# Performance work log

Hardware: AMD Instinct MI355X
Metric: run time of the kernel (lower is better)

Reference implementation:

```python
import jax, jax.numpy as jnp
import numpy as np

N_NODES = 200000
N_EVENTS = 100000
MEM_DIM = 100
TIME_DIM = 100
MSG_DIM = 172
T_MAX = 1000000


def setup_inputs() -> dict:
    key = jax.random.key(0)
    ks = jax.random.split(key, 12)
    s = 0.05
    return {
        "memory": jax.random.normal(ks[0], (N_NODES, MEM_DIM), jnp.float32),
        "raw_msg": jax.random.normal(ks[1], (N_EVENTS, MSG_DIM), jnp.float32),
        "time_w": jax.random.normal(ks[2], (TIME_DIM, 1), jnp.float32) * s,
        "time_b": jax.random.normal(ks[3], (TIME_DIM,), jnp.float32) * s,
        "w_ih": jax.random.normal(ks[4], (3 * MEM_DIM, 2 * MEM_DIM + MSG_DIM + TIME_DIM), jnp.float32) * s,
        "w_hh": jax.random.normal(ks[5], (3 * MEM_DIM, MEM_DIM), jnp.float32) * s,
        "b_ih": jax.random.normal(ks[6], (3 * MEM_DIM,), jnp.float32) * s,
        "b_hh": jax.random.normal(ks[7], (3 * MEM_DIM,), jnp.float32) * s,
        "last_update": jax.random.randint(ks[8], (N_NODES,), 0, T_MAX, jnp.int32),
        "src": jax.random.randint(ks[9], (N_EVENTS,), 0, N_NODES, jnp.int32),
        "dst": jax.random.randint(ks[10], (N_EVENTS,), 0, N_NODES, jnp.int32),
        "t": jax.random.randint(ks[11], (N_EVENTS,), 0, T_MAX, jnp.int32),
    }


def _time_enc(t_rel, time_w, time_b):
    # Linear(1, time_dim) followed by cos, as in TGN.update_memory
    return jnp.cos(t_rel[:, None] * time_w[:, 0][None, :] + time_b[None, :])


def _gru_cell(x, h, w_ih, w_hh, b_ih, b_hh):
    gi = x @ w_ih.T + b_ih  # [N, 3*D]
    gh = h @ w_hh.T + b_hh
    i_r, i_z, i_n = jnp.split(gi, 3, axis=-1)
    h_r, h_z, h_n = jnp.split(gh, 3, axis=-1)
    r = jax.nn.sigmoid(i_r + h_r)
    z = jax.nn.sigmoid(i_z + h_z)
    n = jnp.tanh(i_n + r * h_n)
    return (1.0 - z) * n + z * h


def reference(memory, raw_msg, time_w, time_b, w_ih, w_hh, b_ih, b_hh,
              last_update, src, dst, t):
    # time-relative encodings for source- and destination-side messages
    t_rel_s = (t - last_update[src]).astype(memory.dtype)
    t_rel_d = (t - last_update[dst]).astype(memory.dtype)
    t_enc_s = _time_enc(t_rel_s, time_w, time_b)  # [E, time_dim]
    t_enc_d = _time_enc(t_rel_d, time_w, time_b)

    mem_s = memory[src]  # [E, D]
    mem_d = memory[dst]

    # IdentityMessage: concat(mem_self, mem_other, raw_msg, t_enc)
    msg_s = jnp.concatenate([mem_s, mem_d, raw_msg, t_enc_s], axis=-1)  # [E, 472]
    msg_d = jnp.concatenate([mem_d, mem_s, raw_msg, t_enc_d], axis=-1)

    idx = jnp.concatenate([src, dst], axis=0)          # [2E]
    msgs = jnp.concatenate([msg_s, msg_d], axis=0)      # [2E, 472]

    n_nodes = memory.shape[0]
    # MeanAggregator: per-node mean of incoming messages
    summed = jax.ops.segment_sum(msgs, idx, num_segments=n_nodes)  # [N, 472]
    counts = jax.ops.segment_sum(jnp.ones((idx.shape[0],), memory.dtype), idx,
                                 num_segments=n_nodes)             # [N]
    aggr = summed / jnp.maximum(counts, 1.0)[:, None]

    # GRU memory update, applied only to nodes that received messages
    h_new = _gru_cell(aggr, memory, w_ih, w_hh, b_ih, b_hh)
    touched = (counts > 0)[:, None]
    return jnp.where(touched, h_new, memory)  # [N, memory_dim]
```

## Files before the change

kernel.cpp:

```cpp
#include <hip/hip_runtime.h>
#include <math.h>

#define NND 200000
#define NEV 100000
#define MD 100
#define TD 100
#define MSGD 172
#define NB 64
#define NFRAG 25
#define KS 15
#define BP_ELEMS (KS * NFRAG * 64 * 8)
#define GLS 74

typedef __attribute__((ext_vector_type(8))) short bf16x8;
typedef __attribute__((ext_vector_type(4))) float f32x4;

__device__ __forceinline__ float fast_sigmoid(float x) {
    return 1.0f / (1.0f + __expf(-x));
}
__device__ __forceinline__ float fast_tanh(float x) {
    return fmaf(2.0f, 1.0f / (1.0f + __expf(-2.0f * x)), -1.0f);
}

__device__ __forceinline__ unsigned short f2bf(float f) {
    union { float f; unsigned int u; } v; v.f = f;
    unsigned int r = (v.u + 0x7FFFu + ((v.u >> 16) & 1u)) >> 16;
    return (unsigned short)r;
}
__device__ __forceinline__ float bf2f(unsigned int h) {
    union { unsigned int u; float f; } v; v.u = h << 16;
    return v.f;
}
__device__ __forceinline__ unsigned int pk(float a, float b) {
    unsigned int r;
    asm("v_cvt_pk_bf16_f32 %0, %1, %2" : "=v"(r) : "v"(a), "v"(b));
    return r;
}

__global__ __launch_bounds__(256) void k_count(
    const int* __restrict__ src, const int* __restrict__ dst, int* __restrict__ cnt)
{
    int e = blockIdx.x * 256 + threadIdx.x;
    if (e >= NEV) return;
    atomicAdd(&cnt[src[e]], 1);
    atomicAdd(&cnt[dst[e]], 1);
}

__global__ __launch_bounds__(256) void k_scan1(
    const int* __restrict__ cnt, int* __restrict__ off, int* __restrict__ tpos,
    int* __restrict__ psum, int* __restrict__ psumC)
{
    __shared__ int s[5][256];
    int t = threadIdx.x, b = blockIdx.x;
    int i0 = b * 1024 + t * 4;
    int v[4], cls[4];
#pragma unroll
    for (int j = 0; j < 4; ++j) {
        v[j] = (i0 + j < NND) ? cnt[i0 + j] : 0;
        cls[j] = (v[j] == 0) ? -1 : ((v[j] < 4 ? v[j] : 4) - 1);
    }
    int tsum = v[0] + v[1] + v[2] + v[3];
    int fs[4] = {0, 0, 0, 0};
#pragma unroll
    for (int j = 0; j < 4; ++j)
        if (cls[j] >= 0) fs[cls[j]]++;
    s[0][t] = tsum;
#pragma unroll
    for (int X = 0; X < 4; ++X) s[1 + X][t] = fs[X];
    __syncthreads();
    for (int o = 1; o < 256; o <<= 1) {
        int x[5];
#pragma unroll
        for (int ch = 0; ch < 5; ++ch) x[ch] = (t >= o) ? s[ch][t - o] : 0;
        __syncthreads();
#pragma unroll
        for (int ch = 0; ch < 5; ++ch) s[ch][t] += x[ch];
        __syncthreads();
    }
    int e0 = s[0][t] - tsum;
    int eC[4];
#pragma unroll
    for (int X = 0; X < 4; ++X) eC[X] = s[1 + X][t] - fs[X];
    int run = 0;
    int cseen[4] = {0, 0, 0, 0};
#pragma unroll
    for (int j = 0; j < 4; ++j) {
        int i = i0 + j;
        if (i < NND) {
            off[i] = e0 + run;
            if (cls[j] >= 0) tpos[i] = eC[cls[j]] + cseen[cls[j]];
        }
        run += v[j];
        if (cls[j] >= 0) cseen[cls[j]]++;
    }
    if (t == 255) {
        psum[b] = s[0][255];
#pragma unroll
        for (int X = 0; X < 4; ++X) psumC[X * 256 + b] = s[1 + X][255];
    }
}

__global__ __launch_bounds__(256) void k_scan2(
    int* __restrict__ psum, int* __restrict__ psumC,
    int* __restrict__ clsBase, int* __restrict__ ntp, int nblk)
{
    __shared__ int s[5][256];
    int t = threadIdx.x;
    int v[5];
    v[0] = (t < nblk) ? psum[t] : 0;
#pragma unroll
    for (int X = 0; X < 4; ++X) v[1 + X] = (t < nblk) ? psumC[X * 256 + t] : 0;
#pragma unroll
    for (int ch = 0; ch < 5; ++ch) s[ch][t] = v[ch];
    __syncthreads();
    for (int o = 1; o < 256; o <<= 1) {
        int x[5];
#pragma unroll
        for (int ch = 0; ch < 5; ++ch) x[ch] = (t >= o) ? s[ch][t - o] : 0;
        __syncthreads();
#pragma unroll
        for (int ch = 0; ch < 5; ++ch) s[ch][t] += x[ch];
        __syncthreads();
    }
    if (t < nblk) {
        psum[t] = s[0][t] - v[0];
#pragma unroll
        for (int X = 0; X < 4; ++X) psumC[X * 256 + t] = s[1 + X][t] - v[1 + X];
    }
    if (t == 0) {
        int T0 = s[1][nblk - 1], T1 = s[2][nblk - 1];
        int T2 = s[3][nblk - 1], T3 = s[4][nblk - 1];
        clsBase[0] = 0;
        clsBase[1] = T0;
        clsBase[2] = T0 + T1;
        clsBase[3] = T0 + T1 + T2;
        ntp[0] = T0 + T1 + T2 + T3;
    }
}

__global__ __launch_bounds__(256) void k_scan3(
    const int* __restrict__ cnt, int* __restrict__ off, int* __restrict__ tpos,
    const int* __restrict__ psum, const int* __restrict__ psumC,
    const int* __restrict__ clsBase, int* __restrict__ cur)
{
    int t = threadIdx.x, b = blockIdx.x;
    int base = psum[b];
    int i0 = b * 1024 + t * 4;
#pragma unroll
    for (int j = 0; j < 4; ++j) {
        int i = i0 + j;
        if (i < NND) {
            int v = off[i] + base;
            off[i] = v;
            cur[i] = v;
            int c = cnt[i];
            if (c > 0) {
                int cls = (c < 4 ? c : 4) - 1;
                tpos[i] = clsBase[cls] + psumC[cls * 256 + b] + tpos[i];
            }
        }
    }
}

__global__ __launch_bounds__(256) void k_copytouch(
    const float* __restrict__ memory, const int* __restrict__ cnt,
    const int* __restrict__ off, const int* __restrict__ tpos,
    float* __restrict__ out, int4* __restrict__ tinfo)
{
    int idx = blockIdx.x * 256 + threadIdx.x;
    if (idx >= NND * 25) return;
    int node = idx / 25, u = idx - node * 25;
    int c = cnt[node];
    if (c == 0) {
        reinterpret_cast<float4*>(out)[idx] =
            reinterpret_cast<const float4*>(memory)[idx];
    } else if (u == 0) {
        tinfo[tpos[node]] = make_int4(node, c, off[node], 0);
    }
}

__global__ __launch_bounds__(256) void k_place(
    const int* __restrict__ src, const int* __restrict__ dst,
    const int* __restrict__ tarr, const int* __restrict__ last_update,
    int* __restrict__ cur, int4* __restrict__ entries)
{
    int e = blockIdx.x * 256 + threadIdx.x;
    if (e >= NEV) return;
    int s = src[e], d = dst[e], tt = tarr[e];
    int slot = atomicAdd(&cur[s], 1);
    entries[slot] = make_int4(d, e, __float_as_int((float)(tt - last_update[s])), s);
    slot = atomicAdd(&cur[d], 1);
    entries[slot] = make_int4(s, e, __float_as_int((float)(tt - last_update[d])), d);
}

__global__ __launch_bounds__(256) void k_convert(
    const float* __restrict__ w_ih, const float* __restrict__ w_hh,
    const float* __restrict__ memory, const float* __restrict__ raw_msg,
    unsigned short* __restrict__ Bp, uint4* __restrict__ membf,
    uint4* __restrict__ rawbf)
{
    int idx = blockIdx.x * 256 + threadIdx.x;
    if (idx < BP_ELEMS) {
        int e = idx & 7;
        int lane = (idx >> 3) & 63;
        int t = idx >> 9;
        int nf = t % 25;
        int ks = t / 25;
        int col = nf * 16 + (lane & 15);
        int k = ks * 32 + ((lane >> 4) << 3) + e;
        float v = 0.0f;
        if (col < 200) {
            if (k < 472) v = w_ih[col * 472 + k];
            if (k < 100) v += w_hh[col * 100 + k];
        } else if (col < 300) {
            if (k < 472) v = w_ih[col * 472 + k];
        } else {
            if (k < 100) v = w_hh[(col - 100) * 100 + k];
        }
        Bp[idx] = f2bf(v);
        return;
    }
    int j = idx - BP_ELEMS;
    if (j < NND * 13) {
        int node = j / 13, u = j - node * 13;
        const float4* ms = reinterpret_cast<const float4*>(memory + (size_t)node * MD);
        uint4 o = (uint4){0u, 0u, 0u, 0u};
        if (u < 12) {
            float4 x = ms[2 * u], y = ms[2 * u + 1];
            o.x = pk(x.x, x.y); o.y = pk(x.z, x.w);
            o.z = pk(y.x, y.y); o.w = pk(y.z, y.w);
        } else {
            float4 x = ms[24];
            o.x = pk(x.x, x.y); o.y = pk(x.z, x.w);
        }
        membf[j] = o;
        return;
    }
    j -= NND * 13;
    if (j < NEV * 22) {
        int e = j / 22, r = j - e * 22;
        const float4* rs = reinterpret_cast<const float4*>(raw_msg + (size_t)e * MSGD);
        float4 x = rs[2 * r];
        float4 y = (float4){0.f, 0.f, 0.f, 0.f};
        if (2 * r + 1 < 43) y = rs[2 * r + 1];
        uint4 o;
        o.x = pk(x.x, x.y); o.y = pk(x.z, x.w);
        o.z = pk(y.x, y.y); o.w = pk(y.z, y.w);
        rawbf[j] = o;
    }
}

__global__ __launch_bounds__(512, 4) void tgn_gemm(
    const uint4* __restrict__ membf,
    const uint4* __restrict__ rawbf, const int4* __restrict__ entries,
    const float* __restrict__ time_w, const float* __restrict__ time_b,
    const unsigned short* __restrict__ Bp,
    const float* __restrict__ b_ih, const float* __restrict__ b_hh,
    const int* __restrict__ ntp, const int4* __restrict__ tinfo,
    float* __restrict__ out)
{
    __shared__ __align__(16) unsigned short lds[64 * 480];
    __shared__ int node_s[NB], cnt_s[NB], off_s[NB];
    int tid = threadIdx.x;
    int n0 = blockIdx.x * NB;
    int nt = ntp[0];
    if (n0 >= nt) return;

    if (tid < NB) {
        int slot = n0 + tid;
        if (slot < nt) {
            int4 ti = tinfo[slot];
            node_s[tid] = ti.x; cnt_s[tid] = ti.y; off_s[tid] = ti.z;
        } else {
            node_s[tid] = -1; cnt_s[tid] = 0; off_s[tid] = 0;
        }
    }
    __syncthreads();

    int lane = tid & 63;
    int wv = tid >> 6;

    {
        int u = lane;
        bool lOther = (u >= 13 && u <= 24);
        bool lRaw   = (u >= 25 && u <= 45);
        bool lMix   = (u == 12);
        bool lR46   = (u == 46);
        bool lTenc  = (u >= 47 && u <= 58);
        int offA = lOther ? (16 * u - 200) : (16 * u - 400);

        float tw[8], tb[8];
#pragma unroll
        for (int j = 0; j < 8; ++j) { tw[j] = 0.f; tb[j] = 0.f; }
        if (lTenc) {
            int d0 = 8 * u - 372;
            float4 wa = *reinterpret_cast<const float4*>(time_w + d0);
            float4 wb = *reinterpret_cast<const float4*>(time_w + d0 + 4);
            float4 ba = *reinterpret_cast<const float4*>(time_b + d0);
            float4 bb = *reinterpret_cast<const float4*>(time_b + d0 + 4);
            tw[0] = wa.x; tw[1] = wa.y; tw[2] = wa.z; tw[3] = wa.w;
            tw[4] = wb.x; tw[5] = wb.y; tw[6] = wb.z; tw[7] = wb.w;
            tb[0] = ba.x; tb[1] = ba.y; tb[2] = ba.z; tb[3] = ba.w;
            tb[4] = bb.x; tb[5] = bb.y; tb[6] = bb.z; tb[7] = bb.w;
        } else if (lR46) {
            float4 wa = *reinterpret_cast<const float4*>(time_w);
            float4 ba = *reinterpret_cast<const float4*>(time_b);
            tw[4] = wa.x; tw[5] = wa.y; tw[6] = wa.z; tw[7] = wa.w;
            tb[4] = ba.x; tb[5] = ba.y; tb[6] = ba.z; tb[7] = ba.w;
        }

        const char* membc = reinterpret_cast<const char*>(membf);
        const char* rawbc = reinterpret_cast<const char*>(rawbf);

#pragma unroll
        for (int half = 0; half < 2; ++half) {
            int rb = wv * 8 + half * 4;
            int cc[4], oo[4];
#pragma unroll
            for (int r = 0; r < 4; ++r) { cc[r] = cnt_s[rb + r]; oo[r] = off_s[rb + r]; }
            int maxc = max(max(cc[0], cc[1]), max(cc[2], cc[3]));
            int4 en[4];
#pragma unroll
            for (int r = 0; r < 4; ++r)
                en[r] = (cc[r] > 0) ? entries[oo[r]] : make_int4(0, 0, 0, 0);
            uint4 mreg[4];
#pragma unroll
            for (int r = 0; r < 4; ++r) {
                int nd = node_s[rb + r];
                mreg[r] = (u < 13 && nd >= 0) ? membf[(size_t)nd * 13 + u]
                                              : (uint4){0u, 0u, 0u, 0u};
            }
            uint2 gA[4], gB[4];
#pragma unroll
            for (int r = 0; r < 4; ++r) {
                gA[r] = (uint2){0u, 0u}; gB[r] = (uint2){0u, 0u};
                if (cc[r] > 0) {
                    if (lOther) {
                        const char* p = membc + (size_t)en[r].x * 208 + offA;
                        gA[r] = *reinterpret_cast<const uint2*>(p);
                        gB[r] = *reinterpret_cast<const uint2*>(p + 8);
                    } else if (lMix) {
                        gB[r] = *reinterpret_cast<const uint2*>(membc + (size_t)en[r].x * 208);
                    } else if (lRaw) {
                        const char* p = rawbc + (size_t)en[r].y * 352 + offA;
                        gA[r] = *reinterpret_cast<const uint2*>(p);
                        gB[r] = *reinterpret_cast<const uint2*>(p + 8);
                    } else if (lR46) {
                        gA[r] = *reinterpret_cast<const uint2*>(rawbc + (size_t)en[r].y * 352 + 336);
                    }
                }
            }
            float ac[4][8];
#pragma unroll
            for (int r = 0; r < 4; ++r) {
                ac[r][0] = bf2f(gA[r].x & 0xffffu); ac[r][1] = bf2f(gA[r].x >> 16);
                ac[r][2] = bf2f(gA[r].y & 0xffffu); ac[r][3] = bf2f(gA[r].y >> 16);
                ac[r][4] = bf2f(gB[r].x & 0xffffu); ac[r][5] = bf2f(gB[r].x >> 16);
                ac[r][6] = bf2f(gB[r].y & 0xffffu); ac[r][7] = bf2f(gB[r].y >> 16);
                if ((lTenc || lR46) && cc[r] > 0) {
                    float trel = __int_as_float(en[r].z);
                    if (lTenc) {
                        ac[r][0] = __cosf(fmaf(trel, tw[0], tb[0]));
                        ac[r][1] = __cosf(fmaf(trel, tw[1], tb[1]));
                        ac[r][2] = __cosf(fmaf(trel, tw[2], tb[2]));
                        ac[r][3] = __cosf(fmaf(trel, tw[3], tb[3]));
                    }
                    ac[r][4] = __cosf(fmaf(trel, tw[4], tb[4]));
                    ac[r][5] = __cosf(fmaf(trel, tw[5], tb[5]));
                    ac[r][6] = __cosf(fmaf(trel, tw[6], tb[6]));
                    ac[r][7] = __cosf(fmaf(trel, tw[7], tb[7]));
                }
            }
            for (int j = 1; j < maxc; ++j) {
                int4 e2[4];
#pragma unroll
                for (int r = 0; r < 4; ++r) {
                    int slot = oo[r] + ((j < cc[r]) ? j : 0);
                    e2[r] = entries[slot];
                }
                uint2 hA[4], hB[4];
#pragma unroll
                for (int r = 0; r < 4; ++r) {
                    hA[r] = (uint2){0u, 0u}; hB[r] = (uint2){0u, 0u};
                    if (j < cc[r]) {
                        if (lOther) {
                            const char* p = membc + (size_t)e2[r].x * 208 + offA;
                            hA[r] = *reinterpret_cast<const uint2*>(p);
                            hB[r] = *reinterpret_cast<const uint2*>(p + 8);
                        } else if (lMix) {
                            hB[r] = *reinterpret_cast<const uint2*>(membc + (size_t)e2[r].x * 208);
                        } else if (lRaw) {
                            const char* p = rawbc + (size_t)e2[r].y * 352 + offA;
                            hA[r] = *reinterpret_cast<const uint2*>(p);
                            hB[r] = *reinterpret_cast<const uint2*>(p + 8);
                        } else if (lR46) {
                            hA[r] = *reinterpret_cast<const uint2*>(rawbc + (size_t)e2[r].y * 352 + 336);
                        }
                    }
                }
#pragma unroll
                for (int r = 0; r < 4; ++r) {
                    if (j < cc[r]) {
                        ac[r][0] += bf2f(hA[r].x & 0xffffu); ac[r][1] += bf2f(hA[r].x >> 16);
                        ac[r][2] += bf2f(hA[r].y & 0xffffu); ac[r][3] += bf2f(hA[r].y >> 16);
                        ac[r][4] += bf2f(hB[r].x & 0xffffu); ac[r][5] += bf2f(hB[r].x >> 16);
                        ac[r][6] += bf2f(hB[r].y & 0xffffu); ac[r][7] += bf2f(hB[r].y >> 16);
                        if (lTenc || lR46) {
                            float trel = __int_as_float(e2[r].z);
                            if (lTenc) {
                                ac[r][0] += __cosf(fmaf(trel, tw[0], tb[0]));
                                ac[r][1] += __cosf(fmaf(trel, tw[1], tb[1]));
                                ac[r][2] += __cosf(fmaf(trel, tw[2], tb[2]));
                                ac[r][3] += __cosf(fmaf(trel, tw[3], tb[3]));
                            }
                            ac[r][4] += __cosf(fmaf(trel, tw[4], tb[4]));
                            ac[r][5] += __cosf(fmaf(trel, tw[5], tb[5]));
                            ac[r][6] += __cosf(fmaf(trel, tw[6], tb[6]));
                            ac[r][7] += __cosf(fmaf(trel, tw[7], tb[7]));
                        }
                    }
                }
            }
#pragma unroll
            for (int r = 0; r < 4; ++r) {
                float ci = 1.0f / fmaxf((float)cc[r], 1.0f);
                uint4 o;
                if (u < 12) {
                    o = mreg[r];
                } else {
                    o.x = (u == 12) ? mreg[r].x : pk(ac[r][0] * ci, ac[r][1] * ci);
                    o.y = (u == 12) ? mreg[r].y : pk(ac[r][2] * ci, ac[r][3] * ci);
                    o.z = pk(ac[r][4] * ci, ac[r][5] * ci);
                    o.w = pk(ac[r][6] * ci, ac[r][7] * ci);
                }
                if (u < 60) {
                    int nl = rb + r;
                    int byte = (nl * 960 + 16 * u) ^ ((nl & 7) << 4);
                    *reinterpret_cast<uint4*>(reinterpret_cast<char*>(lds) + byte) = o;
                }
            }
        }
    }
    __syncthreads();

    int l15 = lane & 15;
    int kg8 = (lane >> 4) << 3;
    int f0 = (wv == 0) ? 0 : (4 + 3 * (wv - 1));
    int cw = (wv == 0) ? 4 : 3;

    f32x4 acc[4][4];
#pragma unroll
    for (int g = 0; g < 4; ++g)
#pragma unroll
        for (int i = 0; i < 4; ++i) acc[g][i] = (f32x4){0.f, 0.f, 0.f, 0.f};

    const bf16x8* BpB = reinterpret_cast<const bf16x8*>(Bp);
    const char* ldsc = reinterpret_cast<const char*>(lds);

#pragma unroll
    for (int ks = 0; ks < KS; ++ks) {
        int k0 = ks * 32 + kg8;
        const bf16x8* bp = BpB + ((size_t)(ks * NFRAG + f0)) * 64 + lane;
        bf16x8 b[4];
#pragma unroll
        for (int i = 0; i < 4; ++i)
            if (i < cw) b[i] = bp[i * 64];
#pragma unroll
        for (int g = 0; g < 4; ++g) {
            int r = g * 16 + l15;
            int ab = (r * 960 + 2 * k0) ^ ((r & 7) << 4);
            bf16x8 a = *reinterpret_cast<const bf16x8*>(ldsc + ab);
#pragma unroll
            for (int i = 0; i < 4; ++i)
                if (i < cw)
                    acc[g][i] = __builtin_amdgcn_mfma_f32_16x16x32_bf16(a, b[i], acc[g][i], 0, 0, 0);
        }
    }

    float mv[13];
    {
        const char* membc = reinterpret_cast<const char*>(membf);
#pragma unroll
        for (int t = 0; t < 13; ++t) {
            int idx = tid + t * 512;
            mv[t] = 0.f;
            if (idx < NB * MD) {
                int n = idx / MD, j = idx - n * MD;
                int nd = node_s[n];
                if (nd >= 0) {
                    unsigned short h = *reinterpret_cast<const unsigned short*>(
                        membc + (size_t)nd * 208 + 2 * j);
                    mv[t] = bf2f((unsigned int)h);
                }
            }
        }
    }

    __syncthreads();

    unsigned short* Gl = lds;
    int kq = (lane >> 4) << 2;
#pragma unroll
    for (int i = 0; i < 4; ++i) {
        if (i < cw) {
            int col = (f0 + i) * 16 + l15;
            float bias = (col < 200) ? (b_ih[col] + b_hh[col])
                       : (col < 300) ? b_ih[col] : b_hh[col - 100];
#pragma unroll
            for (int g = 0; g < 4; ++g) {
                int node = g * 16 + kq;
#pragma unroll
                for (int rp = 0; rp < 2; ++rp) {
                    *reinterpret_cast<unsigned int*>(&Gl[col * GLS + node + 2 * rp]) =
                        pk(acc[g][i][2 * rp] + bias, acc[g][i][2 * rp + 1] + bias);
                }
            }
        }
    }
    __syncthreads();

#pragma unroll
    for (int t = 0; t < 13; ++t) {
        int idx = tid + t * 512;
        if (idx < NB * MD) {
            int n = idx / MD, j = idx - n * MD;
            int nd = node_s[n];
            if (nd >= 0) {
                float rp = bf2f((unsigned int)Gl[j * GLS + n]);
                float zp = bf2f((unsigned int)Gl[(100 + j) * GLS + n]);
                float inp = bf2f((unsigned int)Gl[(200 + j) * GLS + n]);
                float hnp = bf2f((unsigned int)Gl[(300 + j) * GLS + n]);
                float r = fast_sigmoid(rp);
                float z = fast_sigmoid(zp);
                float nn = fast_tanh(fmaf(r, hnp, inp));
                float h = (1.0f - z) * nn + z * mv[t];
                out[(size_t)nd * MD + j] = h;
            }
        }
    }
}

extern "C" void kernel_launch(void* const* d_in, const int* in_sizes, int n_in,
                              void* d_out, int out_size, void* d_ws, size_t ws_size,
                              hipStream_t stream)
{
    const float* memory      = (const float*)d_in[0];
    const float* raw_msg     = (const float*)d_in[1];
    const float* time_w      = (const float*)d_in[2];
    const float* time_b      = (const float*)d_in[3];
    const float* w_ih        = (const float*)d_in[4];
    const float* w_hh        = (const float*)d_in[5];
    const float* b_ih        = (const float*)d_in[6];
    const float* b_hh        = (const float*)d_in[7];
    const int*   last_update = (const int*)d_in[8];
    const int*   src         = (const int*)d_in[9];
    const int*   dst         = (const int*)d_in[10];
    const int*   tarr        = (const int*)d_in[11];
    float* out = (float*)d_out;

    int* cnt     = (int*)d_ws;
    int* off     = cnt + NND;
    int* cur     = off + NND;
    int* tpos    = cur + NND;
    int* psum    = tpos + NND;
    int* psumC   = psum + 256;
    int* clsBase = psumC + 1024;
    int* ntp     = clsBase + 4;
    int4* entries = (int4*)(ntp + 4);
    int4* tinfo = entries + 2 * NEV;
    uint4* membf = (uint4*)(tinfo + NND);
    uint4* rawbf = membf + (size_t)NND * 13;
    unsigned short* Bp = (unsigned short*)(rawbf + (size_t)NEV * 22);
    size_t need = (size_t)((char*)(Bp + BP_ELEMS) - (char*)d_ws);
    if (ws_size < need) return;

    const int NBLK = (NND + 1023) / 1024;
    const int NTILE = NND / NB;
    const int CVT_TOTAL = BP_ELEMS + NND * 13 + NEV * 22;

    hipMemsetAsync(cnt, 0, NND * sizeof(int), stream);
    k_convert<<<(CVT_TOTAL + 255) / 256, 256, 0, stream>>>(w_ih, w_hh, memory, raw_msg,
                                                           Bp, membf, rawbf);
    k_count<<<(NEV + 255) / 256, 256, 0, stream>>>(src, dst, cnt);
    k_scan1<<<NBLK, 256, 0, stream>>>(cnt, off, tpos, psum, psumC);
    k_scan2<<<1, 256, 0, stream>>>(psum, psumC, clsBase, ntp, NBLK);
    k_scan3<<<NBLK, 256, 0, stream>>>(cnt, off, tpos, psum, psumC, clsBase, cur);
    k_copytouch<<<(NND * 25 + 255) / 256, 256, 0, stream>>>(memory, cnt, off, tpos, out, tinfo);
    k_place<<<(NEV + 255) / 256, 256, 0, stream>>>(src, dst, tarr, last_update, cur, entries);
    tgn_gemm<<<NTILE, 512, 0, stream>>>(membf, rawbf, entries, time_w, time_b,
                                        Bp, b_ih, b_hh, ntp, tinfo, out);
}
```

Before: 256.6 us.

## Precompute time encodings per entry and merge copy/place kernels

Merges the copy-untouched and place-entries kernels into one launch. Adds a separate kernel that computes the bf16 time encoding for every entry slot, so the GEMM kernel gathers it like the other message parts. The gather code becomes a uniform per-lane source selection, and a fast path for tiles where every node has at most one message writes the gathered bf16 straight to LDS without float accumulation. The cost is an extra launch and 40 MB of extra workspace writes and reads for the encodings.

```diff
diff --git a/kernel.cpp b/kernel.cpp
--- a/kernel.cpp
+++ b/kernel.cpp
@@ -162,35 +162,48 @@
     }
 }
 
-__global__ __launch_bounds__(256) void k_copytouch(
+__global__ __launch_bounds__(256) void k_placecopy(
     const float* __restrict__ memory, const int* __restrict__ cnt,
     const int* __restrict__ off, const int* __restrict__ tpos,
-    float* __restrict__ out, int4* __restrict__ tinfo)
-{
-    int idx = blockIdx.x * 256 + threadIdx.x;
-    if (idx >= NND * 25) return;
-    int node = idx / 25, u = idx - node * 25;
-    int c = cnt[node];
-    if (c == 0) {
-        reinterpret_cast<float4*>(out)[idx] =
-            reinterpret_cast<const float4*>(memory)[idx];
-    } else if (u == 0) {
-        tinfo[tpos[node]] = make_int4(node, c, off[node], 0);
-    }
-}
-
-__global__ __launch_bounds__(256) void k_place(
     const int* __restrict__ src, const int* __restrict__ dst,
     const int* __restrict__ tarr, const int* __restrict__ last_update,
-    int* __restrict__ cur, int4* __restrict__ entries)
-{
-    int e = blockIdx.x * 256 + threadIdx.x;
-    if (e >= NEV) return;
-    int s = src[e], d = dst[e], tt = tarr[e];
-    int slot = atomicAdd(&cur[s], 1);
-    entries[slot] = make_int4(d, e, __float_as_int((float)(tt - last_update[s])), s);
-    slot = atomicAdd(&cur[d], 1);
-    entries[slot] = make_int4(s, e, __float_as_int((float)(tt - last_update[d])), d);
+    int* __restrict__ cur, float* __restrict__ out,
+    int4* __restrict__ tinfo, int4* __restrict__ entries)
+{
+    int idx = blockIdx.x * 256 + threadIdx.x;
+    if (idx < NND * 25) {
+        int node = idx / 25, u = idx - node * 25;
+        int c = cnt[node];
+        if (c == 0) {
+            reinterpret_cast<float4*>(out)[idx] =
+                reinterpret_cast<const float4*>(memory)[idx];
+        } else if (u == 0) {
+            tinfo[tpos[node]] = make_int4(node, c, off[node], 0);
+        }
+        return;
+    }
+    int e = idx - NND * 25;
+    if (e < NEV) {
+        int s = src[e], d = dst[e], tt = tarr[e];
+        int slot = atomicAdd(&cur[s], 1);
+        entries[slot] = make_int4(d, e, __float_as_int((float)(tt - last_update[s])), s);
+        slot = atomicAdd(&cur[d], 1);
+        entries[slot] = make_int4(s, e, __float_as_int((float)(tt - last_update[d])), d);
+    }
+}
+
+__global__ __launch_bounds__(256) void k_tenc(
+    const int4* __restrict__ entries, const float* __restrict__ time_w,
+    const float* __restrict__ time_b, unsigned int* __restrict__ tencbf)
+{
+    int slot = blockIdx.x * 2 + (threadIdx.x >> 7);
+    int k = threadIdx.x & 127;
+    if (k >= 50) return;
+    float trel = __int_as_float(entries[slot].z);
+    float2 w = *reinterpret_cast<const float2*>(time_w + 2 * k);
+    float2 b = *reinterpret_cast<const float2*>(time_b + 2 * k);
+    tencbf[(size_t)slot * 50 + k] =
+        pk(__cosf(fmaf(trel, w.x, b.x)), __cosf(fmaf(trel, w.y, b.y)));
 }
 
 __global__ __launch_bounds__(256) void k_convert(
@@ -251,9 +264,8 @@
 }
 
 __global__ __launch_bounds__(512, 4) void tgn_gemm(
-    const uint4* __restrict__ membf,
-    const uint4* __restrict__ rawbf, const int4* __restrict__ entries,
-    const float* __restrict__ time_w, const float* __restrict__ time_b,
+    const uint4* __restrict__ membf, const uint4* __restrict__ rawbf,
+    const unsigned int* __restrict__ tencbf, const int4* __restrict__ entries,
     const unsigned short* __restrict__ Bp,
     const float* __restrict__ b_ih, const float* __restrict__ b_hh,
     const int* __restrict__ ntp, const int4* __restrict__ tinfo,
@@ -282,35 +294,22 @@
 
     {
         int u = lane;
-        bool lOther = (u >= 13 && u <= 24);
-        bool lRaw   = (u >= 25 && u <= 45);
-        bool lMix   = (u == 12);
-        bool lR46   = (u == 46);
-        bool lTenc  = (u >= 47 && u <= 58);
-        int offA = lOther ? (16 * u - 200) : (16 * u - 400);
-
-        float tw[8], tb[8];
-#pragma unroll
-        for (int j = 0; j < 8; ++j) { tw[j] = 0.f; tb[j] = 0.f; }
-        if (lTenc) {
-            int d0 = 8 * u - 372;
-            float4 wa = *reinterpret_cast<const float4*>(time_w + d0);
-            float4 wb = *reinterpret_cast<const float4*>(time_w + d0 + 4);
-            float4 ba = *reinterpret_cast<const float4*>(time_b + d0);
-            float4 bb = *reinterpret_cast<const float4*>(time_b + d0 + 4);
-            tw[0] = wa.x; tw[1] = wa.y; tw[2] = wa.z; tw[3] = wa.w;
-            tw[4] = wb.x; tw[5] = wb.y; tw[6] = wb.z; tw[7] = wb.w;
-            tb[0] = ba.x; tb[1] = ba.y; tb[2] = ba.z; tb[3] = ba.w;
-            tb[4] = bb.x; tb[5] = bb.y; tb[6] = bb.z; tb[7] = bb.w;
-        } else if (lR46) {
-            float4 wa = *reinterpret_cast<const float4*>(time_w);
-            float4 ba = *reinterpret_cast<const float4*>(time_b);
-            tw[4] = wa.x; tw[5] = wa.y; tw[6] = wa.z; tw[7] = wa.w;
-            tb[4] = ba.x; tb[5] = ba.y; tb[6] = ba.z; tb[7] = ba.w;
-        }
-
         const char* membc = reinterpret_cast<const char*>(membf);
         const char* rawbc = reinterpret_cast<const char*>(rawbf);
+        const char* tencbc = reinterpret_cast<const char*>(tencbf);
+        int selA = 3, selB = 3, strA = 0, strB = 0;
+        const char* bA = membc;
+        const char* bB = membc;
+        if (u == 12) { selB = 0; strB = 208; bB = membc; }
+        else if (u >= 13 && u <= 24) { selA = selB = 0; strA = strB = 208; bA = membc + 16 * u - 200; bB = bA + 8; }
+        else if (u >= 25 && u <= 45) { selA = selB = 1; strA = strB = 352; bA = rawbc + 16 * u - 400; bB = bA + 8; }
+        else if (u == 46) { selA = 1; strA = 352; bA = rawbc + 336; selB = 2; strB = 200; bB = tencbc; }
+        else if (u >= 47 && u <= 58) { selA = selB = 2; strA = strB = 200; bA = tencbc + 16 * u - 744; bB = bA + 8; }
+        bool enA = (selA != 3), enB = (selB != 3);
+
+        auto gidx = [](int sel, int4 e, int slotId) {
+            return (sel == 0) ? e.x : ((sel == 1) ? e.y : slotId);
+        };
 
 #pragma unroll
         for (int half = 0; half < 2; ++half) {
@@ -335,108 +334,80 @@
             for (int r = 0; r < 4; ++r) {
                 gA[r] = (uint2){0u, 0u}; gB[r] = (uint2){0u, 0u};
                 if (cc[r] > 0) {
-                    if (lOther) {
-                        const char* p = membc + (size_t)en[r].x * 208 + offA;
-                        gA[r] = *reinterpret_cast<const uint2*>(p);
-                        gB[r] = *reinterpret_cast<const uint2*>(p + 8);
-                    } else if (lMix) {
-                        gB[r] = *reinterpret_cast<const uint2*>(membc + (size_t)en[r].x * 208);
-                    } else if (lRaw) {
-                        const char* p = rawbc + (size_t)en[r].y * 352 + offA;
-                        gA[r] = *reinterpret_cast<const uint2*>(p);
-                        gB[r] = *reinterpret_cast<const uint2*>(p + 8);
-                    } else if (lR46) {
-                        gA[r] = *reinterpret_cast<const uint2*>(rawbc + (size_t)en[r].y * 352 + 336);
+                    if (enA) gA[r] = *reinterpret_cast<const uint2*>(
+                        bA + (size_t)gidx(selA, en[r], oo[r]) * strA);
+                    if (enB) gB[r] = *reinterpret_cast<const uint2*>(
+                        bB + (size_t)gidx(selB, en[r], oo[r]) * strB);
+                }
+            }
+            if (maxc <= 1) {
+#pragma unroll
+                for (int r = 0; r < 4; ++r) {
+                    uint4 o;
+                    if (u < 12)       o = mreg[r];
+                    else if (u == 12) o = (uint4){mreg[r].x, mreg[r].y, gB[r].x, gB[r].y};
+                    else              o = (uint4){gA[r].x, gA[r].y, gB[r].x, gB[r].y};
+                    if (u < 60) {
+                        int nl = rb + r;
+                        int byte = (nl * 960 + 16 * u) ^ ((nl & 7) << 4);
+                        *reinterpret_cast<uint4*>(reinterpret_cast<char*>(lds) + byte) = o;
                     }
                 }
-            }
-            float ac[4][8];
-#pragma unroll
-            for (int r = 0; r < 4; ++r) {
-                ac[r][0] = bf2f(gA[r].x & 0xffffu); ac[r][1] = bf2f(gA[r].x >> 16);
-                ac[r][2] = bf2f(gA[r].y & 0xffffu); ac[r][3] = bf2f(gA[r].y >> 16);
-                ac[r][4] = bf2f(gB[r].x & 0xffffu); ac[r][5] = bf2f(gB[r].x >> 16);
-                ac[r][6] = bf2f(gB[r].y & 0xffffu); ac[r][7] = bf2f(gB[r].y >> 16);
-                if ((lTenc || lR46) && cc[r] > 0) {
-                    float trel = __int_as_float(en[r].z);
-                    if (lTenc) {
-                        ac[r][0] = __cosf(fmaf(trel, tw[0], tb[0]));
-                        ac[r][1] = __cosf(fmaf(trel, tw[1], tb[1]));
-                        ac[r][2] = __cosf(fmaf(trel, tw[2], tb[2]));
-                        ac[r][3] = __cosf(fmaf(trel, tw[3], tb[3]));
+            } else {
+                float ac[4][8];
+#pragma unroll
+                for (int r = 0; r < 4; ++r) {
+                    ac[r][0] = bf2f(gA[r].x & 0xffffu); ac[r][1] = bf2f(gA[r].x >> 16);
+                    ac[r][2] = bf2f(gA[r].y & 0xffffu); ac[r][3] = bf2f(gA[r].y >> 16);
+                    ac[r][4] = bf2f(gB[r].x & 0xffffu); ac[r][5] = bf2f(gB[r].x >> 16);
+                    ac[r][6] = bf2f(gB[r].y & 0xffffu); ac[r][7] = bf2f(gB[r].y >> 16);
+                }
+                for (int j = 1; j < maxc; ++j) {
+                    int sl[4];
+                    int4 e2[4];
+#pragma unroll
+                    for (int r = 0; r < 4; ++r) {
+                        sl[r] = oo[r] + ((j < cc[r]) ? j : 0);
+                        e2[r] = entries[sl[r]];
                     }
-                    ac[r][4] = __cosf(fmaf(trel, tw[4], tb[4]));
-                    ac[r][5] = __cosf(fmaf(trel, tw[5], tb[5]));
-                    ac[r][6] = __cosf(fmaf(trel, tw[6], tb[6]));
-                    ac[r][7] = __cosf(fmaf(trel, tw[7], tb[7]));
-                }
-            }
-            for (int j = 1; j < maxc; ++j) {
-                int4 e2[4];
-#pragma unroll
-                for (int r = 0; r < 4; ++r) {
-                    int slot = oo[r] + ((j < cc[r]) ? j : 0);
-                    e2[r] = entries[slot];
-                }
-                uint2 hA[4], hB[4];
-#pragma unroll
-                for (int r = 0; r < 4; ++r) {
-                    hA[r] = (uint2){0u, 0u}; hB[r] = (uint2){0u, 0u};
-                    if (j < cc[r]) {
-                        if (lOther) {
-                            const char* p = membc + (size_t)e2[r].x * 208 + offA;
-                            hA[r] = *reinterpret_cast<const uint2*>(p);
-                            hB[r] = *reinterpret_cast<const uint2*>(p + 8);
-                        } else if (lMix) {
-                            hB[r] = *reinterpret_cast<const uint2*>(membc + (size_t)e2[r].x * 208);
-                        } else if (lRaw) {
-                            const char* p = rawbc + (size_t)e2[r].y * 352 + offA;
-                            hA[r] = *reinterpret_cast<const uint2*>(p);
-                            hB[r] = *reinterpret_cast<const uint2*>(p + 8);
-                        } else if (lR46) {
-                            hA[r] = *reinterpret_cast<const uint2*>(rawbc + (size_t)e2[r].y * 352 + 336);
+                    uint2 hA[4], hB[4];
+#pragma unroll
+                    for (int r = 0; r < 4; ++r) {
+                        hA[r] = (uint2){0u, 0u}; hB[r] = (uint2){0u, 0u};
+                        if (j < cc[r]) {
+                            if (enA) hA[r] = *reinterpret_cast<const uint2*>(
+                                bA + (size_t)gidx(selA, e2[r], sl[r]) * strA);
+                            if (enB) hB[r] = *reinterpret_cast<const uint2*>(
+                                bB + (size_t)gidx(selB, e2[r], sl[r]) * strB);
                         }
                     }
-                }
-#pragma unroll
-                for (int r = 0; r < 4; ++r) {
-                    if (j < cc[r]) {
-                        ac[r][0] += bf2f(hA[r].x & 0xffffu); ac[r][1] += bf2f(hA[r].x >> 16);
-                        ac[r][2] += bf2f(hA[r].y & 0xffffu); ac[r][3] += bf2f(hA[r].y >> 16);
-                        ac[r][4] += bf2f(hB[r].x & 0xffffu); ac[r][5] += bf2f(hB[r].x >> 16);
-                        ac[r][6] += bf2f(hB[r].y & 0xffffu); ac[r][7] += bf2f(hB[r].y >> 16);
-                        if (lTenc || lR46) {
-                            float trel = __int_as_float(e2[r].z);
-                            if (lTenc) {
-                                ac[r][0] += __cosf(fmaf(trel, tw[0], tb[0]));
-                                ac[r][1] += __cosf(fmaf(trel, tw[1], tb[1]));
-                                ac[r][2] += __cosf(fmaf(trel, tw[2], tb[2]));
-                                ac[r][3] += __cosf(fmaf(trel, tw[3], tb[3]));
-                            }
-                            ac[r][4] += __cosf(fmaf(trel, tw[4], tb[4]));
-                            ac[r][5] += __cosf(fmaf(trel, tw[5], tb[5]));
-                            ac[r][6] += __cosf(fmaf(trel, tw[6], tb[6]));
-                            ac[r][7] += __cosf(fmaf(trel, tw[7], tb[7]));
+#pragma unroll
+                    for (int r = 0; r < 4; ++r) {
+                        if (j < cc[r]) {
+                            ac[r][0] += bf2f(hA[r].x & 0xffffu); ac[r][1] += bf2f(hA[r].x >> 16);
+                            ac[r][2] += bf2f(hA[r].y & 0xffffu); ac[r][3] += bf2f(hA[r].y >> 16);
+                            ac[r][4] += bf2f(hB[r].x & 0xffffu); ac[r][5] += bf2f(hB[r].x >> 16);
+                            ac[r][6] += bf2f(hB[r].y & 0xffffu); ac[r][7] += bf2f(hB[r].y >> 16);
                         }
                     }
                 }
-            }
-#pragma unroll
-            for (int r = 0; r < 4; ++r) {
-                float ci = 1.0f / fmaxf((float)cc[r], 1.0f);
-                uint4 o;
-                if (u < 12) {
-                    o = mreg[r];
-                } else {
-                    o.x = (u == 12) ? mreg[r].x : pk(ac[r][0] * ci, ac[r][1] * ci);
-                    o.y = (u == 12) ? mreg[r].y : pk(ac[r][2] * ci, ac[r][3] * ci);
-                    o.z = pk(ac[r][4] * ci, ac[r][5] * ci);
-                    o.w = pk(ac[r][6] * ci, ac[r][7] * ci);
-                }
-                if (u < 60) {
-                    int nl = rb + r;
-                    int byte = (nl * 960 + 16 * u) ^ ((nl & 7) << 4);
-                    *reinterpret_cast<uint4*>(reinterpret_cast<char*>(lds) + byte) = o;
+#pragma unroll
+                for (int r = 0; r < 4; ++r) {
+                    float ci = 1.0f / fmaxf((float)cc[r], 1.0f);
+                    uint4 o;
+                    if (u < 12) {
+                        o = mreg[r];
+                    } else {
+                        o.x = (u == 12) ? mreg[r].x : pk(ac[r][0] * ci, ac[r][1] * ci);
+                        o.y = (u == 12) ? mreg[r].y : pk(ac[r][2] * ci, ac[r][3] * ci);
+                        o.z = pk(ac[r][4] * ci, ac[r][5] * ci);
+                        o.w = pk(ac[r][6] * ci, ac[r][7] * ci);
+                    }
+                    if (u < 60) {
+                        int nl = rb + r;
+                        int byte = (nl * 960 + 16 * u) ^ ((nl & 7) << 4);
+                        *reinterpret_cast<uint4*>(reinterpret_cast<char*>(lds) + byte) = o;
+                    }
                 }
             }
         }
@@ -568,7 +539,8 @@
     int* ntp     = clsBase + 4;
     int4* entries = (int4*)(ntp + 4);
     int4* tinfo = entries + 2 * NEV;
-    uint4* membf = (uint4*)(tinfo + NND);
+    unsigned int* tencbf = (unsigned int*)(tinfo + NND);
+    uint4* membf = (uint4*)(tencbf + (size_t)2 * NEV * 50);
     uint4* rawbf = membf + (size_t)NND * 13;
     unsigned short* Bp = (unsigned short*)(rawbf + (size_t)NEV * 22);
     size_t need = (size_t)((char*)(Bp + BP_ELEMS) - (char*)d_ws);
@@ -577,6 +549,7 @@
     const int NBLK = (NND + 1023) / 1024;
     const int NTILE = NND / NB;
     const int CVT_TOTAL = BP_ELEMS + NND * 13 + NEV * 22;
+    const int PC_TOTAL = NND * 25 + NEV;
 
     hipMemsetAsync(cnt, 0, NND * sizeof(int), stream);
     k_convert<<<(CVT_TOTAL + 255) / 256, 256, 0, stream>>>(w_ih, w_hh, memory, raw_msg,
@@ -585,8 +558,10 @@
     k_scan1<<<NBLK, 256, 0, stream>>>(cnt, off, tpos, psum, psumC);
     k_scan2<<<1, 256, 0, stream>>>(psum, psumC, clsBase, ntp, NBLK);
     k_scan3<<<NBLK, 256, 0, stream>>>(cnt, off, tpos, psum, psumC, clsBase, cur);
-    k_copytouch<<<(NND * 25 + 255) / 256, 256, 0, stream>>>(memory, cnt, off, tpos, out, tinfo);
-    k_place<<<(NEV + 255) / 256, 256, 0, stream>>>(src, dst, tarr, last_update, cur, entries);
-    tgn_gemm<<<NTILE, 512, 0, stream>>>(membf, rawbf, entries, time_w, time_b,
+    k_placecopy<<<(PC_TOTAL + 255) / 256, 256, 0, stream>>>(memory, cnt, off, tpos,
+                                                            src, dst, tarr, last_update,
+                                                            cur, out, tinfo, entries);
+    k_tenc<<<NEV, 256, 0, stream>>>(entries, time_w, time_b, tencbf);
+    tgn_gemm<<<NTILE, 512, 0, stream>>>(membf, rawbf, tencbf, entries,
                                         Bp, b_ih, b_hh, ntp, tinfo, out);
 }
```

After: 254.6 us. About the same (-0.8%).
